# Kernel tuning notes

Hardware: AMD Instinct MI355X
Metric: run time of the kernel (lower is better)

The kernel has to match this reference:

```python
import jax, jax.numpy as jnp
import numpy as np

B, C, H, W = 256, 3, 224, 224
RETINA = 32
NUM_ZOOM = 3
SCALE = 2
HG, HL = 1024, 256  # num_hidden_glimpse, num_hidden_location
GDIM = NUM_ZOOM * C * RETINA * RETINA  # 9216


def setup_inputs() -> dict:
    key = jax.random.key(0)
    ks = jax.random.split(key, 12)
    images = jax.random.normal(ks[0], (B, C, H, W), dtype=jnp.float32)
    # locations in [-0.4, 0.4] so all multi-scale crops are in-bounds
    locations = (jax.random.uniform(ks[1], (B, 2), dtype=jnp.float32) * 2.0 - 1.0) * 0.4
    def lin(kw, kb, fan_in, fan_out):
        s = 1.0 / np.sqrt(fan_in)
        Wm = jax.random.uniform(kw, (fan_in, fan_out), jnp.float32, -s, s)
        bm = jax.random.uniform(kb, (fan_out,), jnp.float32, -s, s)
        return Wm, bm
    W1, b1 = lin(ks[2], ks[3], GDIM, HG)
    W2, b2 = lin(ks[4], ks[5], 2, HL)
    W3, b3 = lin(ks[6], ks[7], HG, HG + HL)
    W4, b4 = lin(ks[8], ks[9], HL, HG + HL)
    return {"images": images, "locations": locations,
            "W1": W1, "b1": b1, "W2": W2, "b2": b2,
            "W3": W3, "b3": b3, "W4": W4, "b4": b4}


def _foveate(images, locations):
    # images (B,C,H,W); locations (B,2) in [-1,1]
    denorm = (locations + 1.0) * 0.5 * W  # denormalized pixel coords (row, col)
    zoom_patches = []
    for i in range(NUM_ZOOM):
        half = int(RETINA * 0.5 * SCALE ** i)
        size = 2 * half
        def crop(img, loc):
            # int() truncation == floor for in-bounds (non-negative) offsets
            top = jnp.trunc(loc[0] - half).astype(jnp.int32)
            left = jnp.trunc(loc[1] - half).astype(jnp.int32)
            return jax.lax.dynamic_slice(img, (jnp.int32(0), top, left), (C, size, size))
        crops = jax.vmap(crop)(images, denorm)  # (B,C,size,size)
        resized = jax.image.resize(crops, (crops.shape[0], C, RETINA, RETINA),
                                   method="bilinear", antialias=False)
        zoom_patches.append(resized)
    g = jnp.stack(zoom_patches, axis=1)  # (B, Z, C, r, r)
    return g.reshape(g.shape[0], -1)  # (B, Z*C*r*r)


def reference(images, locations, W1, b1, W2, b2, W3, b3, W4, b4):
    g = _foveate(images, locations)
    hg = jax.nn.relu(jax.nn.relu(g @ W1 + b1) @ W3 + b3)
    hl = jax.nn.relu(jax.nn.relu(locations @ W2 + b2) @ W4 + b4)
    return jax.nn.relu(hg + hl)
```

## Files before the change

### kernel.cpp

```cpp
#include <hip/hip_runtime.h>

typedef __attribute__((ext_vector_type(8))) short short8;
typedef __attribute__((ext_vector_type(16))) float f32x16;

#define Bsz 256
#define Cch 3
#define Him 224
#define Wim 224
#define RET 32
#define HG 1024
#define HL 256
#define GDIM 9216
#define NOUT 1280

__device__ __forceinline__ unsigned short f2bf(float x) {
  unsigned u = __float_as_uint(x);
  return (unsigned short)((u + 0x7fffu + ((u >> 16) & 1u)) >> 16);
}
__device__ __forceinline__ float bf2f(unsigned short h) {
  return __uint_as_float((unsigned)h << 16);
}

__global__ __launch_bounds__(256) void foveate_kernel(
    const float* __restrict__ img, const float* __restrict__ loc,
    unsigned short* __restrict__ ghi, unsigned short* __restrict__ glo) {
  int idx = blockIdx.x * 256 + threadIdx.x;
  int b = idx / GDIM;
  int r = idx - b * GDIM;
  int z = r / (Cch * RET * RET);
  int r2 = r - z * (Cch * RET * RET);
  int c = r2 / (RET * RET);
  int p = r2 - c * (RET * RET);
  int i = p >> 5, j = p & 31;
  float dr = (loc[b * 2 + 0] + 1.f) * .5f * (float)Wim;
  float dc = (loc[b * 2 + 1] + 1.f) * .5f * (float)Wim;
  int half = 16 << z;
  int top = (int)truncf(dr - (float)half), left = (int)truncf(dc - (float)half);
  const float* base = img + ((long)b * Cch + c) * (Him * Wim);
  float v;
  if (z == 0) {
    v = base[(top + i) * Wim + left + j];
  } else {
    int rr = (z == 1) ? top + 2 * i : top + 4 * i + 1;
    int cc = (z == 1) ? left + 2 * j : left + 4 * j + 1;
    v = .25f * (base[rr * Wim + cc] + base[rr * Wim + cc + 1] +
                base[(rr + 1) * Wim + cc] + base[(rr + 1) * Wim + cc + 1]);
  }
  unsigned short h = f2bf(v);
  int off = (r >> 3) * 2048 + b * 8 + (r & 7);
  ghi[off] = h;
  glo[off] = f2bf(v - bf2f(h));
}

__global__ __launch_bounds__(256) void tconv_all_kernel(
    const float* __restrict__ W1, unsigned short* __restrict__ w1h, unsigned short* __restrict__ w1l,
    const float* __restrict__ W3, unsigned short* __restrict__ w3h, unsigned short* __restrict__ w3l,
    const float* __restrict__ W4, unsigned short* __restrict__ w4h, unsigned short* __restrict__ w4l) {
  __shared__ float tile[32][33];
  int bx = blockIdx.x;
  const float* in;
  unsigned short *oh, *ol;
  int K, N, lb;
  if (bx < 9216)       { in = W1; oh = w1h; ol = w1l; K = GDIM; N = HG;   lb = bx; }
  else if (bx < 10496) { in = W3; oh = w3h; ol = w3l; K = HG;   N = NOUT; lb = bx - 9216; }
  else                 { in = W4; oh = w4h; ol = w4l; K = HL;   N = NOUT; lb = bx - 10496; }
  int nb = N >> 5;
  int n0 = (lb % nb) * 32, k0 = (lb / nb) * 32;
  int r = threadIdx.x >> 3, c4 = (threadIdx.x & 7) * 4;
  float4 v = *(const float4*)(in + (long)(k0 + r) * N + n0 + c4);
  tile[r][c4 + 0] = v.x; tile[r][c4 + 1] = v.y;
  tile[r][c4 + 2] = v.z; tile[r][c4 + 3] = v.w;
  __syncthreads();
  if (threadIdx.x < 128) {
    int rr = threadIdx.x >> 2, c8 = (threadIdx.x & 3) * 8;
    unsigned hh[8], ll[8];
#pragma unroll
    for (int j = 0; j < 8; ++j) {
      float x = tile[c8 + j][rr];
      hh[j] = f2bf(x);
      ll[j] = f2bf(x - bf2f((unsigned short)hh[j]));
    }
    long off = (long)((k0 + c8) >> 3) * (N * 8) + (n0 + rr) * 8;
    *(uint4*)(oh + off) = make_uint4(hh[0] | (hh[1] << 16), hh[2] | (hh[3] << 16),
                                     hh[4] | (hh[5] << 16), hh[6] | (hh[7] << 16));
    *(uint4*)(ol + off) = make_uint4(ll[0] | (ll[1] << 16), ll[2] | (ll[3] << 16),
                                     ll[4] | (ll[5] << 16), ll[6] | (ll[7] << 16));
  }
}

__device__ __forceinline__ void gemm_core(
    const unsigned short* __restrict__ Ahi, const unsigned short* __restrict__ Alo,
    int Mtot, int m0,
    const unsigned short* __restrict__ Bhi, const unsigned short* __restrict__ Blo,
    int Ntot, int n0,
    int kblk0, int iters, f32x16 acc[2][2], unsigned short* __restrict__ lds) {
  const int t = threadIdx.x, lane = t & 63;
  const int wm = t >> 7, wn = (t >> 6) & 1;
  const int l5 = lane & 31, lh = lane >> 5;
  unsigned short* lAh = lds;
  unsigned short* lAl = lds + 4096;
  unsigned short* lBh = lds + 8192;
  unsigned short* lBl = lds + 12288;

  long aoff[2], boff[2];
#pragma unroll
  for (int q = 0; q < 2; ++q) {
    int s = q * 256 + t;
    int kb = s >> 7, rr = s & 127;
    aoff[q] = ((long)(kblk0 + kb) * Mtot + m0 + rr) * 8;
    boff[q] = ((long)(kblk0 + kb) * Ntot + n0 + rr) * 8;
  }
  const long da4 = (long)4 * Mtot * 8, db4 = (long)4 * Ntot * 8;
  uint4 rAh[2], rAl[2], rBh[2], rBl[2];
#pragma unroll
  for (int q = 0; q < 2; ++q) {
    rAh[q] = *(const uint4*)(Ahi + aoff[q]);
    rAl[q] = *(const uint4*)(Alo + aoff[q]);
    rBh[q] = *(const uint4*)(Bhi + boff[q]);
    rBl[q] = *(const uint4*)(Blo + boff[q]);
  }

  for (int it = 0; it < iters; ++it) {
    __syncthreads();
#pragma unroll
    for (int q = 0; q < 2; ++q) {
      int d = (q * 256 + t) * 8;
      *(uint4*)(lAh + d) = rAh[q];
      *(uint4*)(lAl + d) = rAl[q];
      *(uint4*)(lBh + d) = rBh[q];
      *(uint4*)(lBl + d) = rBl[q];
    }
    __syncthreads();
    if (it + 1 < iters) {
#pragma unroll
      for (int q = 0; q < 2; ++q) {
        aoff[q] += da4; boff[q] += db4;
        rAh[q] = *(const uint4*)(Ahi + aoff[q]);
        rAl[q] = *(const uint4*)(Alo + aoff[q]);
        rBh[q] = *(const uint4*)(Bhi + boff[q]);
        rBl[q] = *(const uint4*)(Blo + boff[q]);
      }
    }
#pragma unroll
    for (int ks = 0; ks < 2; ++ks) {
      short8 fah[2], fal[2], fbh[2], fbl[2];
#pragma unroll
      for (int mi = 0; mi < 2; ++mi) {
        int off = ((ks * 2 + lh) * 128 + wm * 64 + mi * 32 + l5) * 8;
        fah[mi] = *(const short8*)(lAh + off);
        fal[mi] = *(const short8*)(lAl + off);
      }
#pragma unroll
      for (int ni = 0; ni < 2; ++ni) {
        int off = ((ks * 2 + lh) * 128 + wn * 64 + ni * 32 + l5) * 8;
        fbh[ni] = *(const short8*)(lBh + off);
        fbl[ni] = *(const short8*)(lBl + off);
      }
#pragma unroll
      for (int mi = 0; mi < 2; ++mi)
#pragma unroll
        for (int ni = 0; ni < 2; ++ni)
          acc[mi][ni] = __builtin_amdgcn_mfma_f32_32x32x16_bf16(fah[mi], fbh[ni], acc[mi][ni], 0, 0, 0);
#pragma unroll
      for (int mi = 0; mi < 2; ++mi)
#pragma unroll
        for (int ni = 0; ni < 2; ++ni)
          acc[mi][ni] = __builtin_amdgcn_mfma_f32_32x32x16_bf16(fah[mi], fbl[ni], acc[mi][ni], 0, 0, 0);
#pragma unroll
      for (int mi = 0; mi < 2; ++mi)
#pragma unroll
        for (int ni = 0; ni < 2; ++ni)
          acc[mi][ni] = __builtin_amdgcn_mfma_f32_32x32x16_bf16(fal[mi], fbh[ni], acc[mi][ni], 0, 0, 0);
    }
  }
}

__device__ __forceinline__ void epilogue(float* __restrict__ Pz, int ldp, int m0,
                                         int n0, f32x16 acc[2][2]) {
  const int t = threadIdx.x, lane = t & 63;
  const int wm = t >> 7, wn = (t >> 6) & 1;
  const int l5 = lane & 31, lh = lane >> 5;
#pragma unroll
  for (int mi = 0; mi < 2; ++mi)
#pragma unroll
    for (int ni = 0; ni < 2; ++ni) {
      int col = n0 + wn * 64 + ni * 32 + l5;
      int rbase = m0 + wm * 64 + mi * 32 + 4 * lh;
#pragma unroll
      for (int r = 0; r < 16; ++r) {
        int row = rbase + (r & 3) + 8 * (r >> 2);
        Pz[(long)row * ldp + col] = acc[mi][ni][r];
      }
    }
}

__global__ __launch_bounds__(256, 2) void gemm1_kernel(
    const unsigned short* __restrict__ ghi, const unsigned short* __restrict__ glo,
    const unsigned short* __restrict__ w1h, const unsigned short* __restrict__ w1l,
    float* __restrict__ P) {
  __shared__ __align__(16) unsigned short lds[16384];
  f32x16 acc[2][2];
#pragma unroll
  for (int i = 0; i < 2; ++i)
#pragma unroll
    for (int j = 0; j < 2; ++j)
#pragma unroll
      for (int r = 0; r < 16; ++r) acc[i][j][r] = 0.f;
  int n0 = blockIdx.x * 128, m0 = blockIdx.y * 128, z = blockIdx.z;
  gemm_core(ghi, glo, Bsz, m0, w1h, w1l, HG, n0, z * 36, 9, acc, lds);
  epilogue(P + (long)z * Bsz * HG, HG, m0, n0, acc);
}

__global__ __launch_bounds__(256, 2) void gemm2_kernel(
    const unsigned short* __restrict__ h1h, const unsigned short* __restrict__ h1l,
    const unsigned short* __restrict__ h2h, const unsigned short* __restrict__ h2l,
    const unsigned short* __restrict__ w3h, const unsigned short* __restrict__ w3l,
    const unsigned short* __restrict__ w4h, const unsigned short* __restrict__ w4l,
    float* __restrict__ P) {
  __shared__ __align__(16) unsigned short lds[16384];
  f32x16 acc[2][2];
#pragma unroll
  for (int i = 0; i < 2; ++i)
#pragma unroll
    for (int j = 0; j < 2; ++j)
#pragma unroll
      for (int r = 0; r < 16; ++r) acc[i][j][r] = 0.f;
  int n0 = blockIdx.x * 128, m0 = blockIdx.y * 128, z = blockIdx.z;
  if (z < 16)
    gemm_core(h1h, h1l, Bsz, m0, w3h, w3l, NOUT, n0, z * 8, 2, acc, lds);
  else
    gemm_core(h2h, h2l, Bsz, m0, w4h, w4l, NOUT, n0, (z - 16) * 8, 2, acc, lds);
  epilogue(P + (long)z * Bsz * NOUT, NOUT, m0, n0, acc);
}

__global__ __launch_bounds__(256) void reduce1_h2_kernel(
    const float* __restrict__ P, const float* __restrict__ b1,
    const float* __restrict__ loc, const float* __restrict__ W2,
    const float* __restrict__ b2,
    unsigned short* __restrict__ h1h, unsigned short* __restrict__ h1l,
    unsigned short* __restrict__ h2h, unsigned short* __restrict__ h2l) {
  if (blockIdx.x < 256) {
    int i4 = (blockIdx.x * 256 + threadIdx.x) * 4;
    float4 s = *(const float4*)(P + i4);
    for (int z = 1; z < 32; ++z) {
      float4 p = *(const float4*)(P + (long)z * (Bsz * HG) + i4);
      s.x += p.x; s.y += p.y; s.z += p.z; s.w += p.w;
    }
    int m = i4 >> 10, k = i4 & (HG - 1);
    float4 bb = *(const float4*)(b1 + k);
    float v0 = fmaxf(s.x + bb.x, 0.f), v1 = fmaxf(s.y + bb.y, 0.f);
    float v2 = fmaxf(s.z + bb.z, 0.f), v3 = fmaxf(s.w + bb.w, 0.f);
    unsigned short h0 = f2bf(v0), h1 = f2bf(v1), h2 = f2bf(v2), h3 = f2bf(v3);
    int off = (k >> 3) * 2048 + m * 8 + (k & 7);
    *(ushort4*)(h1h + off) = make_ushort4(h0, h1, h2, h3);
    *(ushort4*)(h1l + off) = make_ushort4(f2bf(v0 - bf2f(h0)), f2bf(v1 - bf2f(h1)),
                                          f2bf(v2 - bf2f(h2)), f2bf(v3 - bf2f(h3)));
  } else {
    int i4 = ((blockIdx.x - 256) * 256 + threadIdx.x) * 4;
    int b = i4 >> 8, k = i4 & (HL - 1);
    float l0 = loc[b * 2 + 0], l1 = loc[b * 2 + 1];
    float4 w0 = *(const float4*)(W2 + k);
    float4 w1 = *(const float4*)(W2 + HL + k);
    float4 bb = *(const float4*)(b2 + k);
    float v0 = fmaxf(fmaf(l0, w0.x, fmaf(l1, w1.x, bb.x)), 0.f);
    float v1 = fmaxf(fmaf(l0, w0.y, fmaf(l1, w1.y, bb.y)), 0.f);
    float v2 = fmaxf(fmaf(l0, w0.z, fmaf(l1, w1.z, bb.z)), 0.f);
    float v3 = fmaxf(fmaf(l0, w0.w, fmaf(l1, w1.w, bb.w)), 0.f);
    unsigned short h0 = f2bf(v0), h1 = f2bf(v1), h2 = f2bf(v2), h3 = f2bf(v3);
    int off = (k >> 3) * 2048 + b * 8 + (k & 7);
    *(ushort4*)(h2h + off) = make_ushort4(h0, h1, h2, h3);
    *(ushort4*)(h2l + off) = make_ushort4(f2bf(v0 - bf2f(h0)), f2bf(v1 - bf2f(h1)),
                                          f2bf(v2 - bf2f(h2)), f2bf(v3 - bf2f(h3)));
  }
}

__global__ __launch_bounds__(256) void reduce2_kernel(
    const float* __restrict__ P, const float* __restrict__ b3,
    const float* __restrict__ b4, float* __restrict__ out) {
  int i4 = (blockIdx.x * 256 + threadIdx.x) * 4;
  const long S = (long)Bsz * NOUT;
  float4 a = *(const float4*)(P + i4);
  for (int z = 1; z < 16; ++z) {
    float4 p = *(const float4*)(P + z * S + i4);
    a.x += p.x; a.y += p.y; a.z += p.z; a.w += p.w;
  }
  float4 c = *(const float4*)(P + 16 * S + i4);
  for (int z = 17; z < 20; ++z) {
    float4 p = *(const float4*)(P + z * S + i4);
    c.x += p.x; c.y += p.y; c.z += p.z; c.w += p.w;
  }
  int n = i4 % NOUT;
  float4 b3v = *(const float4*)(b3 + n);
  float4 b4v = *(const float4*)(b4 + n);
  float4 o;
  o.x = fmaxf(fmaxf(a.x + b3v.x, 0.f) + fmaxf(c.x + b4v.x, 0.f), 0.f);
  o.y = fmaxf(fmaxf(a.y + b3v.y, 0.f) + fmaxf(c.y + b4v.y, 0.f), 0.f);
  o.z = fmaxf(fmaxf(a.z + b3v.z, 0.f) + fmaxf(c.z + b4v.z, 0.f), 0.f);
  o.w = fmaxf(fmaxf(a.w + b3v.w, 0.f) + fmaxf(c.w + b4v.w, 0.f), 0.f);
  *(float4*)(out + i4) = o;
}

extern "C" void kernel_launch(void* const* d_in, const int* in_sizes, int n_in,
                              void* d_out, int out_size, void* d_ws, size_t ws_size,
                              hipStream_t stream) {
  const float* images = (const float*)d_in[0];
  const float* locs = (const float*)d_in[1];
  const float* W1 = (const float*)d_in[2];
  const float* b1 = (const float*)d_in[3];
  const float* W2 = (const float*)d_in[4];
  const float* b2 = (const float*)d_in[5];
  const float* W3 = (const float*)d_in[6];
  const float* b3 = (const float*)d_in[7];
  const float* W4 = (const float*)d_in[8];
  const float* b4 = (const float*)d_in[9];
  float* out = (float*)d_out;

  unsigned short* p = (unsigned short*)d_ws;
  unsigned short* gsh = p; p += 2359296;
  unsigned short* gsl = p; p += 2359296;
  unsigned short* w1h = p; p += 9437184;
  unsigned short* w1l = p; p += 9437184;
  unsigned short* w3h = p; p += 1310720;
  unsigned short* w3l = p; p += 1310720;
  unsigned short* w4h = p; p += 327680;
  unsigned short* w4l = p; p += 327680;
  unsigned short* h1h = p; p += 262144;
  unsigned short* h1l = p; p += 262144;
  unsigned short* h2h = p; p += 65536;
  unsigned short* h2l = p; p += 65536;
  float* P1 = (float*)p;
  float* P2 = P1 + 8388608;

  tconv_all_kernel<<<10816, 256, 0, stream>>>(W1, w1h, w1l, W3, w3h, w3l, W4, w4h, w4l);
  foveate_kernel<<<(Bsz * GDIM) / 256, 256, 0, stream>>>(images, locs, gsh, gsl);
  gemm1_kernel<<<dim3(8, 2, 32), 256, 0, stream>>>(gsh, gsl, w1h, w1l, P1);
  reduce1_h2_kernel<<<320, 256, 0, stream>>>(P1, b1, locs, W2, b2, h1h, h1l, h2h, h2l);
  gemm2_kernel<<<dim3(10, 2, 20), 256, 0, stream>>>(h1h, h1l, h2h, h2l, w3h, w3l, w4h, w4l, P2);
  reduce2_kernel<<<(Bsz * NOUT) / 1024, 256, 0, stream>>>(P2, b3, b4, out);
}
```

Before: 329.2 us.

## Fuse weight bf16 split into GEMM loads, vectorize foveate, fewer split-K slices

Drops the separate weight transpose/convert kernel. The GEMM now loads fp32 weights directly, packs them into hi/lo bf16 in registers with byte-permute truncation, and writes them to LDS through a two-stage register double buffer. The foveate kernel produces four outputs per thread with vector stores, and gemm2 uses fewer, longer split-K slices so reduce2 has fewer partials to sum. This removes a full extra read and write of W1 per call. The cost is strided scalar fp32 weight loads inside the GEMM, more register pressure, and a low part computed by truncation rather than round-to-nearest.

```diff
diff --git a/kernel.cpp b/kernel.cpp
--- a/kernel.cpp
+++ b/kernel.cpp
@@ -24,9 +24,9 @@
 __global__ __launch_bounds__(256) void foveate_kernel(
     const float* __restrict__ img, const float* __restrict__ loc,
     unsigned short* __restrict__ ghi, unsigned short* __restrict__ glo) {
-  int idx = blockIdx.x * 256 + threadIdx.x;
-  int b = idx / GDIM;
-  int r = idx - b * GDIM;
+  int idx4 = (blockIdx.x * 256 + threadIdx.x) * 4;
+  int b = idx4 / GDIM;
+  int r = idx4 - b * GDIM;
   int z = r / (Cch * RET * RET);
   int r2 = r - z * (Cch * RET * RET);
   int c = r2 / (RET * RET);
@@ -37,63 +37,55 @@
   int half = 16 << z;
   int top = (int)truncf(dr - (float)half), left = (int)truncf(dc - (float)half);
   const float* base = img + ((long)b * Cch + c) * (Him * Wim);
-  float v;
+  float v[4];
   if (z == 0) {
-    v = base[(top + i) * Wim + left + j];
+    const float* p0 = base + (top + i) * Wim + left + j;
+#pragma unroll
+    for (int q = 0; q < 4; ++q) v[q] = p0[q];
+  } else if (z == 1) {
+    const float* p0 = base + (top + 2 * i) * Wim + left + 2 * j;
+    const float* p1 = p0 + Wim;
+#pragma unroll
+    for (int q = 0; q < 4; ++q)
+      v[q] = .25f * (p0[2 * q] + p0[2 * q + 1] + p1[2 * q] + p1[2 * q + 1]);
   } else {
-    int rr = (z == 1) ? top + 2 * i : top + 4 * i + 1;
-    int cc = (z == 1) ? left + 2 * j : left + 4 * j + 1;
-    v = .25f * (base[rr * Wim + cc] + base[rr * Wim + cc + 1] +
-                base[(rr + 1) * Wim + cc] + base[(rr + 1) * Wim + cc + 1]);
-  }
-  unsigned short h = f2bf(v);
+    const float* p0 = base + (top + 4 * i + 1) * Wim + left + 4 * j + 1;
+    const float* p1 = p0 + Wim;
+#pragma unroll
+    for (int q = 0; q < 4; ++q)
+      v[q] = .25f * (p0[4 * q] + p0[4 * q + 1] + p1[4 * q] + p1[4 * q + 1]);
+  }
+  unsigned short h[4], l[4];
+#pragma unroll
+  for (int q = 0; q < 4; ++q) {
+    h[q] = f2bf(v[q]);
+    l[q] = f2bf(v[q] - bf2f(h[q]));
+  }
   int off = (r >> 3) * 2048 + b * 8 + (r & 7);
-  ghi[off] = h;
-  glo[off] = f2bf(v - bf2f(h));
-}
-
-__global__ __launch_bounds__(256) void tconv_all_kernel(
-    const float* __restrict__ W1, unsigned short* __restrict__ w1h, unsigned short* __restrict__ w1l,
-    const float* __restrict__ W3, unsigned short* __restrict__ w3h, unsigned short* __restrict__ w3l,
-    const float* __restrict__ W4, unsigned short* __restrict__ w4h, unsigned short* __restrict__ w4l) {
-  __shared__ float tile[32][33];
-  int bx = blockIdx.x;
-  const float* in;
-  unsigned short *oh, *ol;
-  int K, N, lb;
-  if (bx < 9216)       { in = W1; oh = w1h; ol = w1l; K = GDIM; N = HG;   lb = bx; }
-  else if (bx < 10496) { in = W3; oh = w3h; ol = w3l; K = HG;   N = NOUT; lb = bx - 9216; }
-  else                 { in = W4; oh = w4h; ol = w4l; K = HL;   N = NOUT; lb = bx - 10496; }
-  int nb = N >> 5;
-  int n0 = (lb % nb) * 32, k0 = (lb / nb) * 32;
-  int r = threadIdx.x >> 3, c4 = (threadIdx.x & 7) * 4;
-  float4 v = *(const float4*)(in + (long)(k0 + r) * N + n0 + c4);
-  tile[r][c4 + 0] = v.x; tile[r][c4 + 1] = v.y;
-  tile[r][c4 + 2] = v.z; tile[r][c4 + 3] = v.w;
-  __syncthreads();
-  if (threadIdx.x < 128) {
-    int rr = threadIdx.x >> 2, c8 = (threadIdx.x & 3) * 8;
-    unsigned hh[8], ll[8];
-#pragma unroll
-    for (int j = 0; j < 8; ++j) {
-      float x = tile[c8 + j][rr];
-      hh[j] = f2bf(x);
-      ll[j] = f2bf(x - bf2f((unsigned short)hh[j]));
-    }
-    long off = (long)((k0 + c8) >> 3) * (N * 8) + (n0 + rr) * 8;
-    *(uint4*)(oh + off) = make_uint4(hh[0] | (hh[1] << 16), hh[2] | (hh[3] << 16),
-                                     hh[4] | (hh[5] << 16), hh[6] | (hh[7] << 16));
-    *(uint4*)(ol + off) = make_uint4(ll[0] | (ll[1] << 16), ll[2] | (ll[3] << 16),
-                                     ll[4] | (ll[5] << 16), ll[6] | (ll[7] << 16));
-  }
+  *(ushort4*)(ghi + off) = make_ushort4(h[0], h[1], h[2], h[3]);
+  *(ushort4*)(glo + off) = make_ushort4(l[0], l[1], l[2], l[3]);
+}
+
+__device__ __forceinline__ void pack8(const float v[8], uint4& hi, uint4& lo) {
+  unsigned h[4], l[4];
+#pragma unroll
+  for (int p = 0; p < 4; ++p) {
+    unsigned u0 = __float_as_uint(v[2 * p]), u1 = __float_as_uint(v[2 * p + 1]);
+    unsigned m0 = u0 & 0xffff0000u, m1 = u1 & 0xffff0000u;
+    h[p] = __byte_perm(u0, u1, 0x7632);
+    float l0 = v[2 * p] - __uint_as_float(m0);
+    float l1 = v[2 * p + 1] - __uint_as_float(m1);
+    l[p] = __byte_perm(__float_as_uint(l0), __float_as_uint(l1), 0x7632);
+  }
+  hi = make_uint4(h[0], h[1], h[2], h[3]);
+  lo = make_uint4(l[0], l[1], l[2], l[3]);
 }
 
 __device__ __forceinline__ void gemm_core(
     const unsigned short* __restrict__ Ahi, const unsigned short* __restrict__ Alo,
     int Mtot, int m0,
-    const unsigned short* __restrict__ Bhi, const unsigned short* __restrict__ Blo,
-    int Ntot, int n0,
-    int kblk0, int iters, f32x16 acc[2][2], unsigned short* __restrict__ lds) {
+    const float* __restrict__ Bf, int Ntot, int n0,
+    int kb0, int iters, f32x16 acc[2][2], unsigned short* __restrict__ lds) {
   const int t = threadIdx.x, lane = t & 63;
   const int wm = t >> 7, wn = (t >> 6) & 1;
   const int l5 = lane & 31, lh = lane >> 5;
@@ -102,44 +94,62 @@
   unsigned short* lBh = lds + 8192;
   unsigned short* lBl = lds + 12288;
 
-  long aoff[2], boff[2];
+  const int kblk0 = kb0 >> 3;
+  long aoff[2];
 #pragma unroll
   for (int q = 0; q < 2; ++q) {
     int s = q * 256 + t;
-    int kb = s >> 7, rr = s & 127;
-    aoff[q] = ((long)(kblk0 + kb) * Mtot + m0 + rr) * 8;
-    boff[q] = ((long)(kblk0 + kb) * Ntot + n0 + rr) * 8;
-  }
-  const long da4 = (long)4 * Mtot * 8, db4 = (long)4 * Ntot * 8;
-  uint4 rAh[2], rAl[2], rBh[2], rBl[2];
-#pragma unroll
-  for (int q = 0; q < 2; ++q) {
-    rAh[q] = *(const uint4*)(Ahi + aoff[q]);
-    rAl[q] = *(const uint4*)(Alo + aoff[q]);
-    rBh[q] = *(const uint4*)(Bhi + boff[q]);
-    rBl[q] = *(const uint4*)(Blo + boff[q]);
-  }
-
+    aoff[q] = ((long)(kblk0 + (s >> 7)) * Mtot + m0 + (s & 127)) * 8;
+  }
+  const long dA = (long)Mtot * 32;
+  const int bn = t & 127, bkh = t >> 7;
+  const float* bptr = Bf + ((long)kb0 + bkh * 16) * Ntot + n0 + bn;
+  const int bslot = (bkh * 2) * 128 + bn;
+
+  uint4 rAh[2][2], rAl[2][2];
+  float rB[2][16];
+#pragma unroll
+  for (int pb = 0; pb < 2; ++pb) {
+    if (pb < iters) {
+#pragma unroll
+      for (int q = 0; q < 2; ++q) {
+        rAh[pb][q] = *(const uint4*)(Ahi + aoff[q] + pb * dA);
+        rAl[pb][q] = *(const uint4*)(Alo + aoff[q] + pb * dA);
+      }
+#pragma unroll
+      for (int jj = 0; jj < 16; ++jj)
+        rB[pb][jj] = bptr[(long)(pb * 32 + jj) * Ntot];
+    }
+  }
+
+#pragma unroll
   for (int it = 0; it < iters; ++it) {
+    const int pb = it & 1;
     __syncthreads();
 #pragma unroll
     for (int q = 0; q < 2; ++q) {
       int d = (q * 256 + t) * 8;
-      *(uint4*)(lAh + d) = rAh[q];
-      *(uint4*)(lAl + d) = rAl[q];
-      *(uint4*)(lBh + d) = rBh[q];
-      *(uint4*)(lBl + d) = rBl[q];
+      *(uint4*)(lAh + d) = rAh[pb][q];
+      *(uint4*)(lAl + d) = rAl[pb][q];
+    }
+#pragma unroll
+    for (int oct = 0; oct < 2; ++oct) {
+      uint4 hi, lo;
+      pack8(&rB[pb][oct * 8], hi, lo);
+      int d = (bslot + oct * 128) * 8;
+      *(uint4*)(lBh + d) = hi;
+      *(uint4*)(lBl + d) = lo;
     }
     __syncthreads();
-    if (it + 1 < iters) {
+    if (it + 2 < iters) {
 #pragma unroll
       for (int q = 0; q < 2; ++q) {
-        aoff[q] += da4; boff[q] += db4;
-        rAh[q] = *(const uint4*)(Ahi + aoff[q]);
-        rAl[q] = *(const uint4*)(Alo + aoff[q]);
-        rBh[q] = *(const uint4*)(Bhi + boff[q]);
-        rBl[q] = *(const uint4*)(Blo + boff[q]);
-      }
+        rAh[pb][q] = *(const uint4*)(Ahi + aoff[q] + (long)(it + 2) * dA);
+        rAl[pb][q] = *(const uint4*)(Alo + aoff[q] + (long)(it + 2) * dA);
+      }
+#pragma unroll
+      for (int jj = 0; jj < 16; ++jj)
+        rB[pb][jj] = bptr[(long)((it + 2) * 32 + jj) * Ntot];
     }
 #pragma unroll
     for (int ks = 0; ks < 2; ++ks) {
@@ -196,7 +206,24 @@
 
 __global__ __launch_bounds__(256, 2) void gemm1_kernel(
     const unsigned short* __restrict__ ghi, const unsigned short* __restrict__ glo,
-    const unsigned short* __restrict__ w1h, const unsigned short* __restrict__ w1l,
+    const float* __restrict__ W1, float* __restrict__ P) {
+  __shared__ __align__(16) unsigned short lds[16384];
+  f32x16 acc[2][2];
+#pragma unroll
+  for (int i = 0; i < 2; ++i)
+#pragma unroll
+    for (int j = 0; j < 2; ++j)
+#pragma unroll
+      for (int r = 0; r < 16; ++r) acc[i][j][r] = 0.f;
+  int n0 = blockIdx.x * 128, m0 = blockIdx.y * 128, z = blockIdx.z;
+  gemm_core(ghi, glo, Bsz, m0, W1, HG, n0, z * 288, 9, acc, lds);
+  epilogue(P + (long)z * Bsz * HG, HG, m0, n0, acc);
+}
+
+__global__ __launch_bounds__(256, 2) void gemm2_kernel(
+    const unsigned short* __restrict__ h1h, const unsigned short* __restrict__ h1l,
+    const unsigned short* __restrict__ h2h, const unsigned short* __restrict__ h2l,
+    const float* __restrict__ W3, const float* __restrict__ W4,
     float* __restrict__ P) {
   __shared__ __align__(16) unsigned short lds[16384];
   f32x16 acc[2][2];
@@ -207,29 +234,10 @@
 #pragma unroll
       for (int r = 0; r < 16; ++r) acc[i][j][r] = 0.f;
   int n0 = blockIdx.x * 128, m0 = blockIdx.y * 128, z = blockIdx.z;
-  gemm_core(ghi, glo, Bsz, m0, w1h, w1l, HG, n0, z * 36, 9, acc, lds);
-  epilogue(P + (long)z * Bsz * HG, HG, m0, n0, acc);
-}
-
-__global__ __launch_bounds__(256, 2) void gemm2_kernel(
-    const unsigned short* __restrict__ h1h, const unsigned short* __restrict__ h1l,
-    const unsigned short* __restrict__ h2h, const unsigned short* __restrict__ h2l,
-    const unsigned short* __restrict__ w3h, const unsigned short* __restrict__ w3l,
-    const unsigned short* __restrict__ w4h, const unsigned short* __restrict__ w4l,
-    float* __restrict__ P) {
-  __shared__ __align__(16) unsigned short lds[16384];
-  f32x16 acc[2][2];
-#pragma unroll
-  for (int i = 0; i < 2; ++i)
-#pragma unroll
-    for (int j = 0; j < 2; ++j)
-#pragma unroll
-      for (int r = 0; r < 16; ++r) acc[i][j][r] = 0.f;
-  int n0 = blockIdx.x * 128, m0 = blockIdx.y * 128, z = blockIdx.z;
-  if (z < 16)
-    gemm_core(h1h, h1l, Bsz, m0, w3h, w3l, NOUT, n0, z * 8, 2, acc, lds);
+  if (z < 8)
+    gemm_core(h1h, h1l, Bsz, m0, W3, NOUT, n0, z * 128, 4, acc, lds);
   else
-    gemm_core(h2h, h2l, Bsz, m0, w4h, w4l, NOUT, n0, (z - 16) * 8, 2, acc, lds);
+    gemm_core(h2h, h2l, Bsz, m0, W4, NOUT, n0, (z - 8) * 128, 4, acc, lds);
   epilogue(P + (long)z * Bsz * NOUT, NOUT, m0, n0, acc);
 }
 
@@ -280,23 +288,20 @@
   int i4 = (blockIdx.x * 256 + threadIdx.x) * 4;
   const long S = (long)Bsz * NOUT;
   float4 a = *(const float4*)(P + i4);
-  for (int z = 1; z < 16; ++z) {
+  for (int z = 1; z < 8; ++z) {
     float4 p = *(const float4*)(P + z * S + i4);
     a.x += p.x; a.y += p.y; a.z += p.z; a.w += p.w;
   }
-  float4 c = *(const float4*)(P + 16 * S + i4);
-  for (int z = 17; z < 20; ++z) {
-    float4 p = *(const float4*)(P + z * S + i4);
-    c.x += p.x; c.y += p.y; c.z += p.z; c.w += p.w;
-  }
+  float4 c8 = *(const float4*)(P + 8 * S + i4);
+  float4 c9 = *(const float4*)(P + 9 * S + i4);
   int n = i4 % NOUT;
   float4 b3v = *(const float4*)(b3 + n);
   float4 b4v = *(const float4*)(b4 + n);
   float4 o;
-  o.x = fmaxf(fmaxf(a.x + b3v.x, 0.f) + fmaxf(c.x + b4v.x, 0.f), 0.f);
-  o.y = fmaxf(fmaxf(a.y + b3v.y, 0.f) + fmaxf(c.y + b4v.y, 0.f), 0.f);
-  o.z = fmaxf(fmaxf(a.z + b3v.z, 0.f) + fmaxf(c.z + b4v.z, 0.f), 0.f);
-  o.w = fmaxf(fmaxf(a.w + b3v.w, 0.f) + fmaxf(c.w + b4v.w, 0.f), 0.f);
+  o.x = fmaxf(fmaxf(a.x + b3v.x, 0.f) + fmaxf(c8.x + c9.x + b4v.x, 0.f), 0.f);
+  o.y = fmaxf(fmaxf(a.y + b3v.y, 0.f) + fmaxf(c8.y + c9.y + b4v.y, 0.f), 0.f);
+  o.z = fmaxf(fmaxf(a.z + b3v.z, 0.f) + fmaxf(c8.z + c9.z + b4v.z, 0.f), 0.f);
+  o.w = fmaxf(fmaxf(a.w + b3v.w, 0.f) + fmaxf(c8.w + c9.w + b4v.w, 0.f), 0.f);
   *(float4*)(out + i4) = o;
 }
 
@@ -318,12 +323,6 @@
   unsigned short* p = (unsigned short*)d_ws;
   unsigned short* gsh = p; p += 2359296;
   unsigned short* gsl = p; p += 2359296;
-  unsigned short* w1h = p; p += 9437184;
-  unsigned short* w1l = p; p += 9437184;
-  unsigned short* w3h = p; p += 1310720;
-  unsigned short* w3l = p; p += 1310720;
-  unsigned short* w4h = p; p += 327680;
-  unsigned short* w4l = p; p += 327680;
   unsigned short* h1h = p; p += 262144;
   unsigned short* h1l = p; p += 262144;
   unsigned short* h2h = p; p += 65536;
@@ -331,10 +330,9 @@
   float* P1 = (float*)p;
   float* P2 = P1 + 8388608;
 
-  tconv_all_kernel<<<10816, 256, 0, stream>>>(W1, w1h, w1l, W3, w3h, w3l, W4, w4h, w4l);
-  foveate_kernel<<<(Bsz * GDIM) / 256, 256, 0, stream>>>(images, locs, gsh, gsl);
-  gemm1_kernel<<<dim3(8, 2, 32), 256, 0, stream>>>(gsh, gsl, w1h, w1l, P1);
+  foveate_kernel<<<2304, 256, 0, stream>>>(images, locs, gsh, gsl);
+  gemm1_kernel<<<dim3(8, 2, 32), 256, 0, stream>>>(gsh, gsl, W1, P1);
   reduce1_h2_kernel<<<320, 256, 0, stream>>>(P1, b1, locs, W2, b2, h1h, h1l, h2h, h2l);
-  gemm2_kernel<<<dim3(10, 2, 20), 256, 0, stream>>>(h1h, h1l, h2h, h2l, w3h, w3l, w4h, w4l, P2);
-  reduce2_kernel<<<(Bsz * NOUT) / 1024, 256, 0, stream>>>(P2, b3, b4, out);
-}
+  gemm2_kernel<<<dim3(10, 2, 10), 256, 0, stream>>>(h1h, h1l, h2h, h2l, W3, W4, P2);
+  reduce2_kernel<<<320, 256, 0, stream>>>(P2, b3, b4, out);
+}
```

Result: faster. 307.2 us (-6.7%).
